# Performance work log

Measured on AMD Instinct MI355X. Metric: run time of the kernel, lower is better.

## Reference

```python
import jax, jax.numpy as jnp
import numpy as np

DT = 1e-3   # time step [s] (geometry.dt)
H = 10.0    # grid spacing [m] (geometry.h)

# Staggered-grid first differences (2nd-order accurate on the staggered grid).
# Periodic wrap at the boundary via roll; the damping layer d absorbs there.

def _dplus(f, ax):
    return (jnp.roll(f, -1, axis=ax) - f) / H

def _dminus(f, ax):
    return (f - jnp.roll(f, 1, axis=ax)) / H


def setup_inputs() -> dict:
    key = jax.random.key(0)
    ks = jax.random.split(key, 9)
    B, NZ, NX = 4, 2048, 2048
    vp = 1500.0 + 2500.0 * jax.random.uniform(ks[0], (NZ, NX), jnp.float32)   # P velocity [m/s]
    vs = vp / 1.73                                                            # S velocity (Poisson solid)
    rho = 1000.0 + 1000.0 * jax.random.uniform(ks[1], (NZ, NX), jnp.float32)  # density [kg/m^3]
    fields = {}
    for i, name in enumerate(['vx', 'vz', 'txx', 'tzz', 'txz']):
        fields[name] = 1e-3 * jax.random.normal(ks[2 + i], (B, NZ, NX), jnp.float32)
    d = 50.0 * jax.random.uniform(ks[8], (NZ, NX), jnp.float32)               # PML damping profile
    return dict(vp=vp, vs=vs, rho=rho, **fields, d=d)


def reference(vp, vs, rho, vx, vz, txx, tzz, txz, d):
    # Lame parameters from (vp, vs, rho)
    mu = rho * vs * vs
    lam = rho * vp * vp - 2.0 * mu
    # Split-free damping update: y = (1-c)/(1+c) * y_old + dt/(1+c) * rhs
    c = 0.5 * DT * d            # [nz, nx], broadcasts over shot dim
    a = (1.0 - c) / (1.0 + c)
    b = DT / (1.0 + c)
    # --- velocity update (leapfrog: uses old stresses) ---
    vx_new = a * vx + b * (_dminus(txx, -1) + _dminus(txz, -2)) / rho
    vz_new = a * vz + b * (_dplus(txz, -1) + _dplus(tzz, -2)) / rho
    # --- stress update (uses new velocities) ---
    vx_x = _dplus(vx_new, -1)
    vz_z = _dminus(vz_new, -2)
    txx_new = a * txx + b * ((lam + 2.0 * mu) * vx_x + lam * vz_z)
    tzz_new = a * tzz + b * ((lam + 2.0 * mu) * vz_z + lam * vx_x)
    txz_new = a * txz + b * mu * (_dplus(vx_new, -2) + _dminus(vz_new, -1))
    # hidden state for next time step: [5, B, nz, nx]
    return jnp.stack([vx_new, vz_new, txx_new, tzz_new, txz_new])
```

## Files before the change

kernel.cpp:

```cpp
#include <hip/hip_runtime.h>


constexpr int NZ = 2048;
constexpr int NX = 2048;
constexpr int B  = 4;
constexpr int PLANE = NZ * NX;
constexpr int VOL   = B * PLANE;
constexpr float DT    = 1e-3f;
constexpr float INV_H = 0.1f;

__device__ __forceinline__ float rcpf(float x) { return __builtin_amdgcn_rcpf(x); }

__device__ __forceinline__ float vx_new_at(
    const float* __restrict__ txx, const float* __restrict__ txz,
    const float* __restrict__ vx,  const float* __restrict__ rho,
    const float* __restrict__ dd, int b3, int z, int x)
{
    const int zm = (z - 1) & (NZ - 1);
    const int xm = (x - 1) & (NX - 1);
    const int i2 = z * NX + x;
    const int i3 = b3 + i2;
    const float c   = 0.5f * DT * dd[i2];
    const float inv = rcpf(1.0f + c);
    const float a   = (1.0f - c) * inv;
    const float bb  = DT * inv;
    const float rhs = (txx[i3] - txx[b3 + z * NX + xm])
                    + (txz[i3] - txz[b3 + zm * NX + x]);
    return a * vx[i3] + bb * rhs * INV_H * rcpf(rho[i2]);
}

__device__ __forceinline__ float vz_new_at(
    const float* __restrict__ tzz, const float* __restrict__ txz,
    const float* __restrict__ vz,  const float* __restrict__ rho,
    const float* __restrict__ dd, int b3, int z, int x)
{
    const int zp = (z + 1) & (NZ - 1);
    const int xp = (x + 1) & (NX - 1);
    const int i2 = z * NX + x;
    const int i3 = b3 + i2;
    const float c   = 0.5f * DT * dd[i2];
    const float inv = rcpf(1.0f + c);
    const float a   = (1.0f - c) * inv;
    const float bb  = DT * inv;
    const float rhs = (txz[b3 + z * NX + xp] - txz[i3])
                    + (tzz[b3 + zp * NX + x] - tzz[i3]);
    return a * vz[i3] + bb * rhs * INV_H * rcpf(rho[i2]);
}

__global__ __launch_bounds__(256) void wave_fused(
    const float* __restrict__ vp,  const float* __restrict__ vs,
    const float* __restrict__ rho,
    const float* __restrict__ vx,  const float* __restrict__ vz,
    const float* __restrict__ txx, const float* __restrict__ tzz,
    const float* __restrict__ txz,
    const float* __restrict__ dd,
    float* __restrict__ out)
{
    const int i = blockIdx.x * blockDim.x + threadIdx.x;
    if (i >= VOL) return;
    const int x  = i & (NX - 1);
    const int z  = (i >> 11) & (NZ - 1);
    const int b  = i >> 22;
    const int b3 = b * PLANE;
    const int zm = (z - 1) & (NZ - 1);
    const int zp = (z + 1) & (NZ - 1);
    const int xm = (x - 1) & (NX - 1);
    const int xp = (x + 1) & (NX - 1);

    const float vxn_c  = vx_new_at(txx, txz, vx, rho, dd, b3, z,  x);
    const float vxn_xp = vx_new_at(txx, txz, vx, rho, dd, b3, z,  xp);
    const float vxn_zp = vx_new_at(txx, txz, vx, rho, dd, b3, zp, x);
    const float vzn_c  = vz_new_at(tzz, txz, vz, rho, dd, b3, z,  x);
    const float vzn_zm = vz_new_at(tzz, txz, vz, rho, dd, b3, zm, x);
    const float vzn_xm = vz_new_at(tzz, txz, vz, rho, dd, b3, z,  xm);

    const int i2 = z * NX + x;
    const int i3 = b3 + i2;
    const float rh  = rho[i2];
    const float vpv = vp[i2];
    const float vsv = vs[i2];
    const float mu  = rh * vsv * vsv;
    const float lam = rh * vpv * vpv - 2.0f * mu;
    const float lam2mu = lam + 2.0f * mu;
    const float c   = 0.5f * DT * dd[i2];
    const float inv = rcpf(1.0f + c);
    const float a   = (1.0f - c) * inv;
    const float bb  = DT * inv;

    const float vx_x = (vxn_xp - vxn_c) * INV_H;
    const float vz_z = (vzn_c - vzn_zm) * INV_H;
    const float txxn = a * txx[i3] + bb * (lam2mu * vx_x + lam * vz_z);
    const float tzzn = a * tzz[i3] + bb * (lam2mu * vz_z + lam * vx_x);
    const float txzn = a * txz[i3] + bb * mu
                     * ((vxn_zp - vxn_c) * INV_H + (vzn_c - vzn_xm) * INV_H);

    out[0 * VOL + i3] = vxn_c;
    out[1 * VOL + i3] = vzn_c;
    out[2 * VOL + i3] = txxn;
    out[3 * VOL + i3] = tzzn;
    out[4 * VOL + i3] = txzn;
}

extern "C" void kernel_launch(void* const* d_in, const int* in_sizes, int n_in,
                              void* d_out, int out_size, void* d_ws, size_t ws_size,
                              hipStream_t stream) {
    const float* vp  = (const float*)d_in[0];
    const float* vs  = (const float*)d_in[1];
    const float* rho = (const float*)d_in[2];
    const float* vx  = (const float*)d_in[3];
    const float* vz  = (const float*)d_in[4];
    const float* txx = (const float*)d_in[5];
    const float* tzz = (const float*)d_in[6];
    const float* txz = (const float*)d_in[7];
    const float* dd  = (const float*)d_in[8];
    float* out = (float*)d_out;

    const int threads = 256;
    const int blocks  = VOL / threads;
    hipLaunchKernelGGL(wave_fused, dim3(blocks), dim3(threads), 0, stream,
                       vp, vs, rho, vx, vz, txx, tzz, txz, dd, out);
}
```

Before: 688.4 us.

## Vectorize stencil to 4 x-points per thread and loop over batch

```diff
diff --git a/kernel.cpp b/kernel.cpp
--- a/kernel.cpp
+++ b/kernel.cpp
@@ -9,45 +9,19 @@
 constexpr float DT    = 1e-3f;
 constexpr float INV_H = 0.1f;
 
+typedef float f32x4 __attribute__((ext_vector_type(4)));
+
 __device__ __forceinline__ float rcpf(float x) { return __builtin_amdgcn_rcpf(x); }
-
-__device__ __forceinline__ float vx_new_at(
-    const float* __restrict__ txx, const float* __restrict__ txz,
-    const float* __restrict__ vx,  const float* __restrict__ rho,
-    const float* __restrict__ dd, int b3, int z, int x)
-{
-    const int zm = (z - 1) & (NZ - 1);
-    const int xm = (x - 1) & (NX - 1);
-    const int i2 = z * NX + x;
-    const int i3 = b3 + i2;
-    const float c   = 0.5f * DT * dd[i2];
-    const float inv = rcpf(1.0f + c);
-    const float a   = (1.0f - c) * inv;
-    const float bb  = DT * inv;
-    const float rhs = (txx[i3] - txx[b3 + z * NX + xm])
-                    + (txz[i3] - txz[b3 + zm * NX + x]);
-    return a * vx[i3] + bb * rhs * INV_H * rcpf(rho[i2]);
-}
-
-__device__ __forceinline__ float vz_new_at(
-    const float* __restrict__ tzz, const float* __restrict__ txz,
-    const float* __restrict__ vz,  const float* __restrict__ rho,
-    const float* __restrict__ dd, int b3, int z, int x)
-{
-    const int zp = (z + 1) & (NZ - 1);
-    const int xp = (x + 1) & (NX - 1);
-    const int i2 = z * NX + x;
-    const int i3 = b3 + i2;
-    const float c   = 0.5f * DT * dd[i2];
-    const float inv = rcpf(1.0f + c);
-    const float a   = (1.0f - c) * inv;
-    const float bb  = DT * inv;
-    const float rhs = (txz[b3 + z * NX + xp] - txz[i3])
-                    + (tzz[b3 + zp * NX + x] - tzz[i3]);
-    return a * vz[i3] + bb * rhs * INV_H * rcpf(rho[i2]);
-}
-
-__global__ __launch_bounds__(256) void wave_fused(
+__device__ __forceinline__ float4 ld4(const float* __restrict__ p) {
+    return *reinterpret_cast<const float4*>(p);
+}
+__device__ __forceinline__ void st_nt4(float* __restrict__ p,
+                                       float a, float b, float c, float d) {
+    f32x4 v = {a, b, c, d};
+    __builtin_nontemporal_store(v, reinterpret_cast<f32x4*>(p));
+}
+
+__global__ __launch_bounds__(256) void wave_fused_v2(
     const float* __restrict__ vp,  const float* __restrict__ vs,
     const float* __restrict__ rho,
     const float* __restrict__ vx,  const float* __restrict__ vz,
@@ -56,49 +30,163 @@
     const float* __restrict__ dd,
     float* __restrict__ out)
 {
-    const int i = blockIdx.x * blockDim.x + threadIdx.x;
-    if (i >= VOL) return;
-    const int x  = i & (NX - 1);
-    const int z  = (i >> 11) & (NZ - 1);
-    const int b  = i >> 22;
-    const int b3 = b * PLANE;
+    const int t  = blockIdx.x * blockDim.x + threadIdx.x;
+    const int xg = (t & (NX / 4 - 1)) << 2;
+    const int z  = t >> 9;
+    const int zp = (z + 1) & (NZ - 1);
     const int zm = (z - 1) & (NZ - 1);
-    const int zp = (z + 1) & (NZ - 1);
-    const int xm = (x - 1) & (NX - 1);
-    const int xp = (x + 1) & (NX - 1);
-
-    const float vxn_c  = vx_new_at(txx, txz, vx, rho, dd, b3, z,  x);
-    const float vxn_xp = vx_new_at(txx, txz, vx, rho, dd, b3, z,  xp);
-    const float vxn_zp = vx_new_at(txx, txz, vx, rho, dd, b3, zp, x);
-    const float vzn_c  = vz_new_at(tzz, txz, vz, rho, dd, b3, z,  x);
-    const float vzn_zm = vz_new_at(tzz, txz, vz, rho, dd, b3, zm, x);
-    const float vzn_xm = vz_new_at(tzz, txz, vz, rho, dd, b3, z,  xm);
-
-    const int i2 = z * NX + x;
-    const int i3 = b3 + i2;
-    const float rh  = rho[i2];
-    const float vpv = vp[i2];
-    const float vsv = vs[i2];
-    const float mu  = rh * vsv * vsv;
-    const float lam = rh * vpv * vpv - 2.0f * mu;
-    const float lam2mu = lam + 2.0f * mu;
-    const float c   = 0.5f * DT * dd[i2];
-    const float inv = rcpf(1.0f + c);
-    const float a   = (1.0f - c) * inv;
-    const float bb  = DT * inv;
-
-    const float vx_x = (vxn_xp - vxn_c) * INV_H;
-    const float vz_z = (vzn_c - vzn_zm) * INV_H;
-    const float txxn = a * txx[i3] + bb * (lam2mu * vx_x + lam * vz_z);
-    const float tzzn = a * tzz[i3] + bb * (lam2mu * vz_z + lam * vx_x);
-    const float txzn = a * txz[i3] + bb * mu
-                     * ((vxn_zp - vxn_c) * INV_H + (vzn_c - vzn_xm) * INV_H);
-
-    out[0 * VOL + i3] = vxn_c;
-    out[1 * VOL + i3] = vzn_c;
-    out[2 * VOL + i3] = txxn;
-    out[3 * VOL + i3] = tzzn;
-    out[4 * VOL + i3] = txzn;
+    const int xm1 = (xg - 1) & (NX - 1);
+    const int xp4 = (xg + 4) & (NX - 1);
+    const int rz  = z  * NX;
+    const int rzp = zp * NX;
+    const int rzm = zm * NX;
+
+    float dz6[6], rz6[6];
+    {
+        const float4 d4 = ld4(dd + rz + xg);
+        dz6[0] = dd[rz + xm1]; dz6[1] = d4.x; dz6[2] = d4.y;
+        dz6[3] = d4.z;         dz6[4] = d4.w; dz6[5] = dd[rz + xp4];
+        const float4 r4 = ld4(rho + rz + xg);
+        rz6[0] = rho[rz + xm1]; rz6[1] = r4.x; rz6[2] = r4.y;
+        rz6[3] = r4.z;          rz6[4] = r4.w; rz6[5] = rho[rz + xp4];
+    }
+    float avz[6], bvz[6], inv_c[4];
+    #pragma unroll
+    for (int j = 0; j < 6; ++j) {
+        const float c   = 0.5f * DT * dz6[j];
+        const float inv = rcpf(1.0f + c);
+        avz[j] = (1.0f - c) * inv;
+        bvz[j] = DT * INV_H * inv * rcpf(rz6[j]);
+        if (j >= 1 && j <= 4) inv_c[j - 1] = inv;
+    }
+    float avzp[4], bvzp[4], avzm[4], bvzm[4];
+    {
+        const float4 dp = ld4(dd + rzp + xg), dm = ld4(dd + rzm + xg);
+        const float4 rp = ld4(rho + rzp + xg), rm = ld4(rho + rzm + xg);
+        const float dpa[4] = {dp.x, dp.y, dp.z, dp.w};
+        const float dma[4] = {dm.x, dm.y, dm.z, dm.w};
+        const float rpa[4] = {rp.x, rp.y, rp.z, rp.w};
+        const float rma[4] = {rm.x, rm.y, rm.z, rm.w};
+        #pragma unroll
+        for (int k = 0; k < 4; ++k) {
+            float c = 0.5f * DT * dpa[k];
+            float inv = rcpf(1.0f + c);
+            avzp[k] = (1.0f - c) * inv;
+            bvzp[k] = DT * INV_H * inv * rcpf(rpa[k]);
+            c = 0.5f * DT * dma[k];
+            inv = rcpf(1.0f + c);
+            avzm[k] = (1.0f - c) * inv;
+            bvzm[k] = DT * INV_H * inv * rcpf(rma[k]);
+        }
+    }
+    float q1[4], q2[4], q3[4], a_s[4];
+    {
+        const float4 vp4 = ld4(vp + rz + xg), vs4 = ld4(vs + rz + xg);
+        const float vpa[4] = {vp4.x, vp4.y, vp4.z, vp4.w};
+        const float vsa[4] = {vs4.x, vs4.y, vs4.z, vs4.w};
+        #pragma unroll
+        for (int k = 0; k < 4; ++k) {
+            const float r   = rz6[k + 1];
+            const float muv = r * vsa[k] * vsa[k];
+            const float lam = r * vpa[k] * vpa[k] - 2.0f * muv;
+            const float bsH = DT * INV_H * inv_c[k];
+            q1[k] = bsH * (lam + 2.0f * muv);
+            q2[k] = bsH * lam;
+            q3[k] = bsH * muv;
+            a_s[k] = avz[k + 1];
+        }
+    }
+
+    #pragma unroll 1
+    for (int b = 0; b < B; ++b) {
+        const int b3  = b * PLANE;
+        const int cz  = b3 + rz  + xg;
+        const int czp = b3 + rzp + xg;
+        const int czm = b3 + rzm + xg;
+
+        float txxz[6], txzz[6], tzzz[5], tzzzp[5], txxzp[5];
+        float txzzm[5];
+        float vxz[5];
+        float vzz[5];
+        {
+            float4 m;
+            m = ld4(txx + cz);
+            txxz[1] = m.x; txxz[2] = m.y; txxz[3] = m.z; txxz[4] = m.w;
+            txxz[0] = txx[b3 + rz + xm1];  txxz[5] = txx[b3 + rz + xp4];
+            m = ld4(txz + cz);
+            txzz[1] = m.x; txzz[2] = m.y; txzz[3] = m.z; txzz[4] = m.w;
+            txzz[0] = txz[b3 + rz + xm1];  txzz[5] = txz[b3 + rz + xp4];
+            m = ld4(tzz + cz);
+            tzzz[1] = m.x; tzzz[2] = m.y; tzzz[3] = m.z; tzzz[4] = m.w;
+            tzzz[0] = tzz[b3 + rz + xm1];
+            m = ld4(tzz + czp);
+            tzzzp[1] = m.x; tzzzp[2] = m.y; tzzzp[3] = m.z; tzzzp[4] = m.w;
+            tzzzp[0] = tzz[b3 + rzp + xm1];
+            m = ld4(txx + czp);
+            txxzp[1] = m.x; txxzp[2] = m.y; txxzp[3] = m.z; txxzp[4] = m.w;
+            txxzp[0] = txx[b3 + rzp + xm1];
+            m = ld4(txz + czm);
+            txzzm[0] = m.x; txzzm[1] = m.y; txzzm[2] = m.z; txzzm[3] = m.w;
+            txzzm[4] = txz[b3 + rzm + xp4];
+            m = ld4(vx + cz);
+            vxz[0] = m.x; vxz[1] = m.y; vxz[2] = m.z; vxz[3] = m.w;
+            vxz[4] = vx[b3 + rz + xp4];
+            m = ld4(vz + cz);
+            vzz[1] = m.x; vzz[2] = m.y; vzz[3] = m.z; vzz[4] = m.w;
+            vzz[0] = vz[b3 + rz + xm1];
+        }
+        const float4 tp4 = ld4(txz + czp);
+        const float4 tm4 = ld4(tzz + czm);
+        const float4 vxp4 = ld4(vx + czp);
+        const float4 vzm4 = ld4(vz + czm);
+        const float txzzp[4] = {tp4.x, tp4.y, tp4.z, tp4.w};
+        const float tzzzm[4] = {tm4.x, tm4.y, tm4.z, tm4.w};
+        const float vxzp[4]  = {vxp4.x, vxp4.y, vxp4.z, vxp4.w};
+        const float vzzm[4]  = {vzm4.x, vzm4.y, vzm4.z, vzm4.w};
+
+        float vxn_z[5];
+        #pragma unroll
+        for (int k = 0; k < 5; ++k)
+            vxn_z[k] = avz[k + 1] * vxz[k]
+                     + bvz[k + 1] * ((txxz[k + 1] - txxz[k])
+                                   + (txzz[k + 1] - txzzm[k]));
+        float vzn_z[5];
+        #pragma unroll
+        for (int k = 0; k < 5; ++k)
+            vzn_z[k] = avz[k] * vzz[k]
+                     + bvz[k] * ((txzz[k + 1] - txzz[k])
+                               + (tzzzp[k] - tzzz[k]));
+        float vxn_zp[4];
+        #pragma unroll
+        for (int k = 0; k < 4; ++k)
+            vxn_zp[k] = avzp[k] * vxzp[k]
+                      + bvzp[k] * ((txxzp[k + 1] - txxzp[k])
+                                 + (txzzp[k] - txzz[k + 1]));
+        float vzn_zm[4];
+        #pragma unroll
+        for (int k = 0; k < 4; ++k)
+            vzn_zm[k] = avzm[k] * vzzm[k]
+                      + bvzm[k] * ((txzzm[k + 1] - txzzm[k])
+                                 + (tzzz[k + 1] - tzzzm[k]));
+
+        float oxx[4], ozz[4], oxz[4];
+        #pragma unroll
+        for (int k = 0; k < 4; ++k) {
+            const float dvx = vxn_z[k + 1] - vxn_z[k];
+            const float dvz = vzn_z[k + 1] - vzn_zm[k];
+            oxx[k] = a_s[k] * txxz[k + 1] + q1[k] * dvx + q2[k] * dvz;
+            ozz[k] = a_s[k] * tzzz[k + 1] + q1[k] * dvz + q2[k] * dvx;
+            oxz[k] = a_s[k] * txzz[k + 1]
+                   + q3[k] * ((vxn_zp[k] - vxn_z[k])
+                            + (vzn_z[k + 1] - vzn_z[k]));
+        }
+
+        st_nt4(out + 0 * VOL + cz, vxn_z[0], vxn_z[1], vxn_z[2], vxn_z[3]);
+        st_nt4(out + 1 * VOL + cz, vzn_z[1], vzn_z[2], vzn_z[3], vzn_z[4]);
+        st_nt4(out + 2 * VOL + cz, oxx[0], oxx[1], oxx[2], oxx[3]);
+        st_nt4(out + 3 * VOL + cz, ozz[0], ozz[1], ozz[2], ozz[3]);
+        st_nt4(out + 4 * VOL + cz, oxz[0], oxz[1], oxz[2], oxz[3]);
+    }
 }
 
 extern "C" void kernel_launch(void* const* d_in, const int* in_sizes, int n_in,
@@ -116,7 +204,7 @@
     float* out = (float*)d_out;
 
     const int threads = 256;
-    const int blocks  = VOL / threads;
-    hipLaunchKernelGGL(wave_fused, dim3(blocks), dim3(threads), 0, stream,
+    const int blocks  = (PLANE / 4) / threads;
+    hipLaunchKernelGGL(wave_fused_v2, dim3(blocks), dim3(threads), 0, stream,
                        vp, vs, rho, vx, vz, txx, tzz, txz, dd, out);
 }
```

Measured after the change: 620.2 us. 9.9% less time.
